# Performance work log

Measured on AMD Instinct MI355X. Metric: run time of the kernel, lower is better.

Reference implementation:

```python
import jax, jax.numpy as jnp
import numpy as np

N_NODES = 50000
N_EDGES = 800000
D_FEAT = 128
HIDDEN = 128
BERT_DIM = 768
BATCH = 4096
MAX_ENT = 20
COMB = BERT_DIM + HIDDEN  # 896


def setup_inputs() -> dict:
    key = jax.random.key(0)
    ks = jax.random.split(key, 12)
    article_bert_embeddings = jax.random.normal(ks[0], (BATCH, BERT_DIM), dtype=jnp.float32)
    x = jax.random.normal(ks[1], (N_NODES, D_FEAT), dtype=jnp.float32)
    edge_index = jax.random.randint(ks[2], (2, N_EDGES), 0, N_NODES, dtype=jnp.int64)
    entity_map = jax.random.randint(ks[3], (BATCH, MAX_ENT), 0, N_NODES, dtype=jnp.int64)
    pad = jax.random.uniform(ks[4], (BATCH, MAX_ENT)) < 0.3
    entity_map = jnp.where(pad, jnp.int64(-1), entity_map)
    s = 1.0 / np.sqrt(D_FEAT)
    W1 = jax.random.normal(ks[5], (D_FEAT, HIDDEN), dtype=jnp.float32) * s
    b1 = jnp.zeros((HIDDEN,), dtype=jnp.float32)
    W2 = jax.random.normal(ks[6], (HIDDEN, HIDDEN), dtype=jnp.float32) * (1.0 / np.sqrt(HIDDEN))
    b2 = jnp.zeros((HIDDEN,), dtype=jnp.float32)
    fc1_w = jax.random.normal(ks[7], (COMB, COMB // 2), dtype=jnp.float32) * (1.0 / np.sqrt(COMB))
    fc1_b = jnp.zeros((COMB // 2,), dtype=jnp.float32)
    fc2_w = jax.random.normal(ks[8], (COMB // 2, 1), dtype=jnp.float32) * (1.0 / np.sqrt(COMB // 2))
    fc2_b = jnp.zeros((1,), dtype=jnp.float32)
    return dict(article_bert_embeddings=article_bert_embeddings, x=x,
                edge_index=edge_index, entity_map=entity_map,
                W1=W1, b1=b1, W2=W2, b2=b2,
                fc1_w=fc1_w, fc1_b=fc1_b, fc2_w=fc2_w, fc2_b=fc2_b)


def _gcn_norm(edge_index, n_nodes):
    # add self loops (PyG GCNConv default) and compute symmetric normalization
    loops = jnp.arange(n_nodes, dtype=edge_index.dtype)
    src = jnp.concatenate([edge_index[0], loops])
    dst = jnp.concatenate([edge_index[1], loops])
    deg = jax.ops.segment_sum(jnp.ones_like(dst, dtype=jnp.float32), dst, num_segments=n_nodes)
    dinv = jnp.where(deg > 0, jax.lax.rsqrt(deg), 0.0)
    norm = dinv[src] * dinv[dst]  # [E+N]
    return src, dst, norm


def _gcn_conv(h, W, b, src, dst, norm, n_nodes):
    h = h @ W                                   # [N, H] transform first (cheaper)
    msg = h[src] * norm[:, None]                # [E+N, H] gather
    out = jax.ops.segment_sum(msg, dst, num_segments=n_nodes)
    return out + b


def reference(article_bert_embeddings, x, edge_index, entity_map,
              W1, b1, W2, b2, fc1_w, fc1_b, fc2_w, fc2_b):
    n = x.shape[0]
    src, dst, norm = _gcn_norm(edge_index, n)
    # GNN (dropout in eval mode = identity)
    h = jax.nn.relu(_gcn_conv(x, W1, b1, src, dst, norm, n))
    h = jax.nn.relu(_gcn_conv(h, W2, b2, src, dst, norm, n))
    # ragged mean over entity lists (-1 = padding), fully vectorized
    mask = entity_map >= 0                           # [B, M]
    safe_ids = jnp.where(mask, entity_map, 0)
    gathered = h[safe_ids] * mask[..., None]         # [B, M, H]
    cnt = jnp.maximum(mask.sum(axis=1, keepdims=True).astype(h.dtype), 1.0)
    batch_gnn = gathered.sum(axis=1) / cnt           # [B, H]; rows w/ no entities stay 0
    combined = jnp.concatenate([article_bert_embeddings, batch_gnn], axis=1)
    z = jax.nn.relu(combined @ fc1_w + fc1_b)
    logits = z @ fc2_w + fc2_b
    return jax.nn.sigmoid(logits)
```

## Files before the change

kernel.cpp:

```cpp
#include <hip/hip_runtime.h>
#include <math.h>

typedef __bf16 bf16_t;
typedef __bf16 bfrag8 __attribute__((ext_vector_type(8)));
typedef float  facc4  __attribute__((ext_vector_type(4)));
typedef float  f32x2  __attribute__((ext_vector_type(2)));

#define NBUCK 512
#define BCAP  4096

__device__ inline unsigned short f2b(float x) {
    unsigned int u = __float_as_uint(x);
    unsigned int r = (u + 0x7fffu + ((u >> 16) & 1u)) >> 16;
    return (unsigned short)r;
}
__device__ inline unsigned int pack2(float lo, float hi) {
    return (unsigned int)f2b(lo) | ((unsigned int)f2b(hi) << 16);
}
__device__ inline float blo(unsigned int q) { return __uint_as_float(q << 16); }
__device__ inline float bhi(unsigned int q) { return __uint_as_float(q & 0xffff0000u); }

#if __has_builtin(__builtin_amdgcn_cvt_pk_f32_fp8) && __has_builtin(__builtin_amdgcn_cvt_pk_fp8_f32)
#define HW_FP8 1
#endif

__device__ inline f32x2 fp8pair_dec(unsigned short v) {
#ifdef HW_FP8
    return __builtin_amdgcn_cvt_pk_f32_fp8((int)(unsigned int)v, false);
#else
    f32x2 r;
    unsigned char b0 = (unsigned char)(v & 0xff), b1 = (unsigned char)(v >> 8);
    {
        int e = (b0 >> 3) & 0xf, m = b0 & 7;
        float mag = e ? ldexpf(8.f + m, e - 10) : ldexpf((float)m, -9);
        r.x = (b0 & 0x80) ? -mag : mag;
    }
    {
        int e = (b1 >> 3) & 0xf, m = b1 & 7;
        float mag = e ? ldexpf(8.f + m, e - 10) : ldexpf((float)m, -9);
        r.y = (b1 & 0x80) ? -mag : mag;
    }
    return r;
#endif
}
__device__ inline unsigned char fp8_enc(float x) {
#ifdef HW_FP8
    return (unsigned char)(__builtin_amdgcn_cvt_pk_fp8_f32(x, x, 0, false) & 0xff);
#else
    unsigned char s = (x < 0.f) ? 0x80 : 0;
    float ax = fabsf(x);
    if (!(ax > 0.f)) return s;
    if (ax >= 448.f) return s | 0x7e;
    if (ax < 0.015625f) {
        int q = (int)rintf(ax * 512.f);
        return s | (unsigned char)q;
    }
    int e; float m = frexpf(ax, &e);
    int q = (int)rintf(m * 16.f);
    int E = e - 1;
    if (q == 16) { q = 8; ++E; }
    if (E > 8) return s | 0x7e;
    return s | (unsigned char)(((E + 7) << 3) | (q - 8));
#endif
}

__device__ inline int bucket_of(int d, int N) {
    return (int)(((long long)d * NBUCK) / N);
}


__device__ inline void bin2_body(char* smem, const int* __restrict__ src,
                                 const int* __restrict__ dst,
                                 int* __restrict__ bcnt,
                                 unsigned int* __restrict__ ebuf,
                                 int E, int N, int bb) {
    unsigned int* sorted = (unsigned int*)smem;
    int* hist   = (int*)(smem + 16384);
    int* lstart = (int*)(smem + 18432);
    int* gbase  = (int*)(smem + 20480);
    int* sm     = (int*)(smem + 22528);
    int tid = threadIdx.x;
    int base = bb * 4096;
    int cnt = min(4096, E - base);
    hist[tid] = 0; hist[tid + 256] = 0;
    __syncthreads();
    unsigned int mye[16]; int myb[16];
#pragma unroll
    for (int i = 0; i < 16; ++i) {
        int idx = i * 256 + tid;
        myb[i] = -1;
        if (idx < cnt) {
            int e = base + idx;
            int s = src[e], d = dst[e];
            mye[i] = ((unsigned int)s << 16) | (unsigned int)d;
            int b = bucket_of(d, N);
            myb[i] = b;
            atomicAdd(&hist[b], 1);
        }
    }
    __syncthreads();
    int p0 = hist[2 * tid], p1 = hist[2 * tid + 1];
    sm[tid] = p0 + p1;
    __syncthreads();
    for (int off = 1; off < 256; off <<= 1) {
        int x = (tid >= off) ? sm[tid - off] : 0;
        __syncthreads();
        sm[tid] += x;
        __syncthreads();
    }
    int excl = sm[tid] - (p0 + p1);
    lstart[2 * tid] = excl;
    lstart[2 * tid + 1] = excl + p0;
    __syncthreads();
    hist[tid] = lstart[tid]; hist[tid + 256] = lstart[tid + 256];
    __syncthreads();
#pragma unroll
    for (int i = 0; i < 16; ++i) {
        if (myb[i] >= 0) {
            int pos = atomicAdd(&hist[myb[i]], 1);
            sorted[pos] = mye[i];
        }
    }
    __syncthreads();
    for (int b = tid; b < NBUCK; b += 256) {
        int c = hist[b] - lstart[b];
        gbase[b] = (c > 0) ? atomicAdd(&bcnt[b], c) : 0;
    }
    __syncthreads();
    for (int idx = tid; idx < cnt; idx += 256) {
        unsigned int v = sorted[idx];
        int b = bucket_of((int)(v & 0xffffu), N);
        ebuf[(size_t)b * BCAP + gbase[b] + (idx - lstart[b])] = v;
    }
}

__device__ inline void build2_body(char* smem, const unsigned int* __restrict__ ebuf,
                                   const int* __restrict__ bcnt,
                                   int* __restrict__ offs,
                                   float* __restrict__ dinv,
                                   unsigned short* __restrict__ csr,
                                   int N, int E, int b) {
    unsigned short* seg = (unsigned short*)smem;
    int* cnt_l  = (int*)(smem + 8192);
    int* scan_l = (int*)(smem + 8704);
    int* curs   = (int*)(smem + 9216);
    int* smr    = (int*)(smem + 9728);
    int tid = threadIdx.x;
    int part = 0;
    for (int j = tid; j < b; j += 256) part += bcnt[j];
    smr[tid] = part;
    __syncthreads();
    for (int off = 128; off > 0; off >>= 1) {
        if (tid < off) smr[tid] += smr[tid + off];
        __syncthreads();
    }
    int base = smr[0];
    int lo = (int)(((long long)b * N + NBUCK - 1) / NBUCK);
    int cnt = bcnt[b];
    int nrange = (int)(((long long)(b + 1) * N + NBUCK - 1) / NBUCK) - lo;
    if (b == 0 && tid == 0) offs[N] = E;
    if (tid < 128) cnt_l[tid] = 0;
    __syncthreads();
    for (int i = tid; i < cnt; i += 256) {
        unsigned int v = ebuf[(size_t)b * BCAP + i];
        atomicAdd(&cnt_l[(int)(v & 0xffffu) - lo], 1);
    }
    __syncthreads();
    if (tid < 128) scan_l[tid] = cnt_l[tid];
    __syncthreads();
    for (int off = 1; off < 128; off <<= 1) {
        int x = 0;
        if (tid < 128 && tid >= off) x = scan_l[tid - off];
        __syncthreads();
        if (tid < 128) scan_l[tid] += x;
        __syncthreads();
    }
    if (tid < 128) {
        int excl = scan_l[tid] - cnt_l[tid];
        curs[tid] = excl;
        if (tid < nrange) {
            offs[lo + tid] = base + excl;
            dinv[lo + tid] = rsqrtf((float)(cnt_l[tid] + 1));
        }
    }
    __syncthreads();
    for (int i = tid; i < cnt; i += 256) {
        unsigned int v = ebuf[(size_t)b * BCAP + i];
        int d = (int)(v & 0xffffu) - lo;
        int p = atomicAdd(&curs[d], 1);
        seg[p] = (unsigned short)(v >> 16);
    }
    __syncthreads();
    for (int i = tid; i < cnt; i += 256) csr[base + i] = seg[i];
}

__device__ inline void gemm1_body(char* smem, const float* __restrict__ A,
                                  const bf16_t* __restrict__ Bt,
                                  unsigned char* __restrict__ out8, int M, int bb) {
    bf16_t* As = (bf16_t*)smem;
    bf16_t* Bs = (bf16_t*)(smem + 17408);
    int t = threadIdx.x;
    int wave = t >> 6, lane = t & 63, quad = lane >> 4, l16 = lane & 15;
    int r0 = bb * 64;
#pragma unroll
    for (int i = 0; i < 4; ++i) {
        int chunk = t + i * 256;
        int row = chunk >> 4, c8 = (chunk & 15) << 3;
        int gr = r0 + row;
        float4 a0 = make_float4(0.f, 0.f, 0.f, 0.f), a1 = a0;
        if (gr < M) {
            a0 = *(const float4*)&A[(size_t)gr * 128 + c8];
            a1 = *(const float4*)&A[(size_t)gr * 128 + c8 + 4];
        }
        *(uint4*)&As[row * 136 + c8] =
            make_uint4(pack2(a0.x, a0.y), pack2(a0.z, a0.w),
                       pack2(a1.x, a1.y), pack2(a1.z, a1.w));
    }
#pragma unroll
    for (int i = 0; i < 8; ++i) {
        int chunk = t + i * 256;
        int row = chunk >> 4, c8 = (chunk & 15) << 3;
        *(uint4*)&Bs[row * 136 + c8] = *(const uint4*)&Bt[row * 128 + c8];
    }
    __syncthreads();

    facc4 acc[8];
#pragma unroll
    for (int nt = 0; nt < 8; ++nt) acc[nt] = (facc4){0.f, 0.f, 0.f, 0.f};
    int arow = (wave << 4) + l16;
#pragma unroll
    for (int ks = 0; ks < 4; ++ks) {
        int kk = ks * 32 + quad * 8;
        bfrag8 af = *(const bfrag8*)&As[arow * 136 + kk];
#pragma unroll
        for (int nt = 0; nt < 8; ++nt) {
            bfrag8 bf = *(const bfrag8*)&Bs[(nt * 16 + l16) * 136 + kk];
            acc[nt] = __builtin_amdgcn_mfma_f32_16x16x32_bf16(af, bf, acc[nt], 0, 0, 0);
        }
    }
    __syncthreads();
    unsigned char* f8t = (unsigned char*)As;
    int wrow0 = (wave << 4) + quad * 4;
#pragma unroll
    for (int r = 0; r < 4; ++r) {
        int row = wrow0 + r;
#pragma unroll
        for (int nt = 0; nt < 8; ++nt)
            f8t[row * 128 + nt * 16 + l16] = fp8_enc(acc[nt][r]);
    }
    __syncthreads();
#pragma unroll
    for (int i = 0; i < 2; ++i) {
        int idx = t + i * 256;
        int row = idx >> 3, cc = (idx & 7) << 4;
        int gr = r0 + row;
        if (gr < M) *(uint4*)&out8[(size_t)gr * 128 + cc] = *(const uint4*)&f8t[row * 128 + cc];
    }
}

__global__ __launch_bounds__(256) void k_bin_gemm(const int* __restrict__ src,
                                                  const int* __restrict__ dst,
                                                  int* __restrict__ bcnt,
                                                  unsigned int* __restrict__ ebuf,
                                                  int E, int N,
                                                  const float* __restrict__ A,
                                                  const bf16_t* __restrict__ Bt,
                                                  unsigned char* __restrict__ out8,
                                                  int nbin) {
    __shared__ __align__(16) char smem[52224];
    if ((int)blockIdx.x < nbin)
        bin2_body(smem, src, dst, bcnt, ebuf, E, N, blockIdx.x);
    else
        gemm1_body(smem, A, Bt, out8, N, blockIdx.x - nbin);
}

__global__ __launch_bounds__(256) void k_build_gemm(const unsigned int* __restrict__ ebuf,
                                                    const int* __restrict__ bcnt,
                                                    int* __restrict__ offs,
                                                    float* __restrict__ dinv,
                                                    unsigned short* __restrict__ csr,
                                                    int N, int E,
                                                    const float* __restrict__ A,
                                                    const bf16_t* __restrict__ Bt,
                                                    unsigned char* __restrict__ out8,
                                                    int tile0) {
    __shared__ __align__(16) char smem[52224];
    if ((int)blockIdx.x < NBUCK)
        build2_body(smem, ebuf, bcnt, offs, dinv, csr, N, E, blockIdx.x);
    else
        gemm1_body(smem, A, Bt, out8, N, blockIdx.x - NBUCK + tile0);
}

__global__ __launch_bounds__(256) void k_prep(const float* __restrict__ bert,
                                              unsigned int* __restrict__ bertb, int n8,
                                              const float* __restrict__ W1,
                                              unsigned short* __restrict__ w1t,
                                              const float* __restrict__ W2,
                                              unsigned short* __restrict__ w2t,
                                              const float* __restrict__ Wf,
                                              unsigned short* __restrict__ fwt,
                                              int* __restrict__ bcnt,
                                              float* __restrict__ logacc) {
    __shared__ float tile[64][65];
    int ncvt = (n8 + 255) / 256;
    int bb = blockIdx.x, tid = threadIdx.x;
    if (bb < ncvt) {
        int i = bb * 256 + tid;
        if (i >= n8) return;
        const float4* p = (const float4*)bert + (size_t)i * 2;
        float4 a = p[0], b = p[1];
        uint4 o;
        o.x = pack2(a.x, a.y);
        o.y = pack2(a.z, a.w);
        o.z = pack2(b.x, b.y);
        o.w = pack2(b.z, b.w);
        ((uint4*)bertb)[i] = o;
        return;
    }
    bb -= ncvt;
    if (bb < 128) {
        int i = bb * 256 + tid;
        const float* W = (i < 16384) ? W1 : W2;
        unsigned short* Wt = (i < 16384) ? w1t : w2t;
        int idx = i & 16383;
        int n = idx >> 7, k = idx & 127;
        Wt[idx] = f2b(W[k * 128 + n]);
        return;
    }
    bb -= 128;
    if (bb < 98) {
        int n0 = (bb % 7) * 64, k0 = (bb / 7) * 64;
#pragma unroll
        for (int i = 0; i < 16; ++i) {
            int idx = i * 256 + tid;
            int r = idx >> 6, c = idx & 63;
            tile[r][c] = Wf[(size_t)(k0 + r) * 448 + n0 + c];
        }
        __syncthreads();
#pragma unroll
        for (int i = 0; i < 16; ++i) {
            int idx = i * 256 + tid;
            int c = idx >> 6, r = idx & 63;
            fwt[(size_t)(n0 + c) * 896 + k0 + r] = f2b(tile[r][c]);
        }
        return;
    }
    if (tid < 256) { bcnt[tid] = 0; bcnt[tid + 256] = 0; }
#pragma unroll
    for (int i = 0; i < 16; ++i) logacc[i * 256 + tid] = 0.f;
}

__global__ __launch_bounds__(256) void k_aggmm(const unsigned short* __restrict__ hx8,
                                               const unsigned short* __restrict__ csr,
                                               const int* __restrict__ offs,
                                               const float* __restrict__ dinv,
                                               const float* __restrict__ bias1,
                                               const bf16_t* __restrict__ W2t,
                                               unsigned char* __restrict__ out8, int N) {
    __shared__ bf16_t As[64 * 136];
    __shared__ bf16_t Bs[128 * 136];
    int t = threadIdx.x;
    int wave = t >> 6, lane = t & 63, quad = lane >> 4, l16 = lane & 15;
    int r0 = blockIdx.x * 64;
#pragma unroll
    for (int i = 0; i < 8; ++i) {
        int chunk = t + i * 256;
        int row = chunk >> 4, c8 = (chunk & 15) << 3;
        *(uint4*)&Bs[row * 136 + c8] = *(const uint4*)&W2t[row * 128 + c8];
    }
    float2 b2v = *(const float2*)&bias1[lane * 2];
    for (int i = 0; i < 16; ++i) {
        int row = (wave << 4) + i;
        int node = r0 + row;
        float v0 = 0.f, v1 = 0.f;
        if (node < N) {
            float di = dinv[node];
            f32x2 sf = fp8pair_dec(hx8[(size_t)node * 64 + lane]);
            float acc0 = sf.x * di, acc1 = sf.y * di;
            int s0 = offs[node], s1 = offs[node + 1];
            for (int eb = s0; eb < s1; eb += 64) {
                int nloc = min(64, s1 - eb);
                int en = 0; float dvl = 0.f;
                if (lane < nloc) { en = (int)csr[eb + lane]; dvl = dinv[en]; }
                int j = 0;
                for (; j + 16 <= nloc; j += 16) {
                    int sid[16]; float dv[16]; unsigned short g[16];
#pragma unroll
                    for (int u = 0; u < 16; ++u) {
                        sid[u] = __shfl(en, j + u, 64);
                        dv[u]  = __shfl(dvl, j + u, 64);
                    }
#pragma unroll
                    for (int u = 0; u < 16; ++u) g[u] = hx8[(size_t)sid[u] * 64 + lane];
#pragma unroll
                    for (int u = 0; u < 16; ++u) {
                        f32x2 d = fp8pair_dec(g[u]);
                        acc0 += d.x * dv[u]; acc1 += d.y * dv[u];
                    }
                }
                for (; j + 4 <= nloc; j += 4) {
                    int sid[4]; float dv[4]; unsigned short g[4];
#pragma unroll
                    for (int u = 0; u < 4; ++u) {
                        sid[u] = __shfl(en, j + u, 64);
                        dv[u]  = __shfl(dvl, j + u, 64);
                    }
#pragma unroll
                    for (int u = 0; u < 4; ++u) g[u] = hx8[(size_t)sid[u] * 64 + lane];
#pragma unroll
                    for (int u = 0; u < 4; ++u) {
                        f32x2 d = fp8pair_dec(g[u]);
                        acc0 += d.x * dv[u]; acc1 += d.y * dv[u];
                    }
                }
                for (; j < nloc; ++j) {
                    int sn = __shfl(en, j, 64);
                    float dv = __shfl(dvl, j, 64);
                    f32x2 d = fp8pair_dec(hx8[(size_t)sn * 64 + lane]);
                    acc0 += d.x * dv; acc1 += d.y * dv;
                }
            }
            v0 = fmaxf(acc0 * di + b2v.x, 0.f);
            v1 = fmaxf(acc1 * di + b2v.y, 0.f);
        }
        *(unsigned int*)&As[row * 136 + lane * 2] = pack2(v0, v1);
    }
    __syncthreads();
    facc4 acc[8];
#pragma unroll
    for (int nt = 0; nt < 8; ++nt) acc[nt] = (facc4){0.f, 0.f, 0.f, 0.f};
    int arow = (wave << 4) + l16;
#pragma unroll
    for (int ks = 0; ks < 4; ++ks) {
        int kk = ks * 32 + quad * 8;
        bfrag8 af = *(const bfrag8*)&As[arow * 136 + kk];
#pragma unroll
        for (int nt = 0; nt < 8; ++nt) {
            bfrag8 bf = *(const bfrag8*)&Bs[(nt * 16 + l16) * 136 + kk];
            acc[nt] = __builtin_amdgcn_mfma_f32_16x16x32_bf16(af, bf, acc[nt], 0, 0, 0);
        }
    }
    __syncthreads();
    unsigned char* f8t = (unsigned char*)As;
    int wrow0 = (wave << 4) + quad * 4;
#pragma unroll
    for (int r = 0; r < 4; ++r) {
        int row = wrow0 + r;
        float sc = dinv[min(r0 + row, N - 1)];
#pragma unroll
        for (int nt = 0; nt < 8; ++nt)
            f8t[row * 128 + nt * 16 + l16] = fp8_enc(acc[nt][r] * sc);
    }
    __syncthreads();
#pragma unroll
    for (int i = 0; i < 2; ++i) {
        int idx = t + i * 256;
        int row = idx >> 3, cc = (idx & 7) << 4;
        int gr = r0 + row;
        if (gr < N) *(uint4*)&out8[(size_t)gr * 128 + cc] = *(const uint4*)&f8t[row * 128 + cc];
    }
}

__global__ __launch_bounds__(256) void k_agg_b(const unsigned short* __restrict__ hx8,
                                               const unsigned short* __restrict__ csr,
                                               const int* __restrict__ offs,
                                               const float* __restrict__ dinv,
                                               const float* __restrict__ bias,
                                               unsigned int* __restrict__ out, int N) {
    int node = blockIdx.x * 4 + (threadIdx.x >> 6);
    int lane = threadIdx.x & 63;
    if (node >= N) return;
    float di = dinv[node];
    f32x2 sf = fp8pair_dec(hx8[(size_t)node * 64 + lane]);
    float acc0 = sf.x, acc1 = sf.y;
    int s0 = offs[node], s1 = offs[node + 1];
    for (int base = s0; base < s1; base += 64) {
        int nloc = min(64, s1 - base);
        int en = 0;
        if (lane < nloc) en = (int)csr[base + lane];
        int j = 0;
        for (; j + 16 <= nloc; j += 16) {
            int sid[16]; unsigned short g[16];
#pragma unroll
            for (int u = 0; u < 16; ++u) sid[u] = __shfl(en, j + u, 64);
#pragma unroll
            for (int u = 0; u < 16; ++u) g[u] = hx8[(size_t)sid[u] * 64 + lane];
#pragma unroll
            for (int u = 0; u < 16; ++u) { f32x2 d = fp8pair_dec(g[u]); acc0 += d.x; acc1 += d.y; }
        }
        for (; j + 4 <= nloc; j += 4) {
            int sid[4]; unsigned short g[4];
#pragma unroll
            for (int u = 0; u < 4; ++u) sid[u] = __shfl(en, j + u, 64);
#pragma unroll
            for (int u = 0; u < 4; ++u) g[u] = hx8[(size_t)sid[u] * 64 + lane];
#pragma unroll
            for (int u = 0; u < 4; ++u) { f32x2 d = fp8pair_dec(g[u]); acc0 += d.x; acc1 += d.y; }
        }
        for (; j < nloc; ++j) {
            int srcn = __shfl(en, j, 64);
            f32x2 d = fp8pair_dec(hx8[(size_t)srcn * 64 + lane]);
            acc0 += d.x; acc1 += d.y;
        }
    }
    float2 bb = *(const float2*)&bias[lane * 2];
    float v0 = fmaxf(acc0 * di + bb.x, 0.f);
    float v1 = fmaxf(acc1 * di + bb.y, 0.f);
    out[(size_t)node * 64 + lane] = pack2(v0, v1);
}

__global__ __launch_bounds__(256) void k_pool_b(const unsigned int* __restrict__ h,
                                                const int* __restrict__ ent,
                                                unsigned int* __restrict__ out) {
    int r = blockIdx.x * 4 + (threadIdx.x >> 6);
    int lane = threadIdx.x & 63;
    float a0 = 0.f, a1 = 0.f;
    int cnt = 0;
#pragma unroll
    for (int m = 0; m < 20; ++m) {
        int id = ent[r * 20 + m];
        if (id >= 0) {
            unsigned int q = h[(size_t)id * 64 + lane];
            a0 += blo(q); a1 += bhi(q); cnt++;
        }
    }
    float inv = 1.f / (float)max(cnt, 1);
    out[(size_t)r * 64 + lane] = pack2(a0 * inv, a1 * inv);
}

__global__ __launch_bounds__(256) void k_mlp1_mfma(const bf16_t* __restrict__ bertb,
                                                   const bf16_t* __restrict__ gnnb,
                                                   const bf16_t* __restrict__ fwt,
                                                   const float* __restrict__ fb,
                                                   const float* __restrict__ w2,
                                                   float* __restrict__ logacc) {
    __shared__ bf16_t As[64 * 136];
    __shared__ bf16_t Bs[64 * 136];
    int t = threadIdx.x;
    int wave = t >> 6, lane = t & 63, quad = lane >> 4, l16 = lane & 15;
    int r0 = blockIdx.x * 64, c0 = blockIdx.y * 64;
    facc4 acc[4];
#pragma unroll
    for (int nt = 0; nt < 4; ++nt) acc[nt] = (facc4){0.f, 0.f, 0.f, 0.f};

    for (int ks = 0; ks < 7; ++ks) {
#pragma unroll
        for (int i = 0; i < 4; ++i) {
            int chunk = t + i * 256;
            int row = chunk >> 4, c8 = (chunk & 15) << 3;
            int gr = r0 + row;
            const bf16_t* srcp = (ks < 6) ? &bertb[(size_t)gr * 768 + ks * 128 + c8]
                                          : &gnnb[(size_t)gr * 128 + c8];
            *(uint4*)&As[row * 136 + c8] = *(const uint4*)srcp;
        }
#pragma unroll
        for (int i = 0; i < 4; ++i) {
            int chunk = t + i * 256;
            int row = chunk >> 4, c8 = (chunk & 15) << 3;
            *(uint4*)&Bs[row * 136 + c8] =
                *(const uint4*)&fwt[(size_t)(c0 + row) * 896 + ks * 128 + c8];
        }
        __syncthreads();
        int arow = (wave << 4) + l16;
#pragma unroll
        for (int sub = 0; sub < 4; ++sub) {
            int kk = sub * 32 + quad * 8;
            bfrag8 af = *(const bfrag8*)&As[arow * 136 + kk];
#pragma unroll
            for (int nt = 0; nt < 4; ++nt) {
                bfrag8 bf = *(const bfrag8*)&Bs[(nt * 16 + l16) * 136 + kk];
                acc[nt] = __builtin_amdgcn_mfma_f32_16x16x32_bf16(af, bf, acc[nt], 0, 0, 0);
            }
        }
        __syncthreads();
    }
    int rbase = r0 + (wave << 4) + quad * 4;
    float part[4] = {0.f, 0.f, 0.f, 0.f};
#pragma unroll
    for (int nt = 0; nt < 4; ++nt) {
        int col = c0 + nt * 16 + l16;
        float bb = fb[col];
        float ww = w2[col];
#pragma unroll
        for (int r = 0; r < 4; ++r)
            part[r] += fmaxf(acc[nt][r] + bb, 0.f) * ww;
    }
#pragma unroll
    for (int m = 8; m >= 1; m >>= 1) {
#pragma unroll
        for (int r = 0; r < 4; ++r) part[r] += __shfl_xor(part[r], m, 64);
    }
    if (l16 == 0) {
#pragma unroll
        for (int r = 0; r < 4; ++r) atomicAdd(&logacc[rbase + r], part[r]);
    }
}

__global__ void k_sig(const float* __restrict__ logacc, const float* __restrict__ b,
                      float* __restrict__ out, int B) {
    int i = blockIdx.x * 256 + threadIdx.x;
    if (i < B) out[i] = 1.f / (1.f + expf(-(logacc[i] + b[0])));
}

extern "C" void kernel_launch(void* const* d_in, const int* in_sizes, int n_in,
                              void* d_out, int out_size, void* d_ws, size_t ws_size,
                              hipStream_t stream) {
    const float* bert = (const float*)d_in[0];
    const float* x    = (const float*)d_in[1];
    const int*   ei   = (const int*)d_in[2];
    const int*   ent  = (const int*)d_in[3];
    const float* W1   = (const float*)d_in[4];
    const float* b1   = (const float*)d_in[5];
    const float* W2   = (const float*)d_in[6];
    const float* b2   = (const float*)d_in[7];
    const float* fc1w = (const float*)d_in[8];
    const float* fc1b = (const float*)d_in[9];
    const float* fc2w = (const float*)d_in[10];
    const float* fc2b = (const float*)d_in[11];
    float* out = (float*)d_out;

    const int N = in_sizes[1] / 128;
    const int E = in_sizes[2] / 2;
    const int B = in_sizes[0] / 768;

    const int* srcv = ei;
    const int* dstv = ei + E;

    char* wsp = (char*)d_ws;
    size_t off = 0;
    auto alloc = [&](size_t bytes) -> void* {
        void* p = wsp + off;
        off += (bytes + 255) & ~(size_t)255;
        return p;
    };
    float* dinv   = (float*)alloc((size_t)N * 4);
    int*   offs   = (int*)alloc((size_t)(N + 1) * 4);
    int*   bcnt   = (int*)alloc(NBUCK * 4);
    float* logacc = (float*)alloc((size_t)B * 4);
    unsigned int*   ebuf  = (unsigned int*)alloc((size_t)NBUCK * BCAP * 4);
    unsigned short* csr16 = (unsigned short*)alloc((size_t)E * 2);
    bf16_t* bertb = (bf16_t*)alloc((size_t)B * 768 * 2);
    bf16_t* w1t   = (bf16_t*)alloc(128 * 128 * 2);
    bf16_t* w2t   = (bf16_t*)alloc(128 * 128 * 2);
    bf16_t* fwt   = (bf16_t*)alloc((size_t)896 * 448 * 2);
    unsigned char* g8a = (unsigned char*)alloc((size_t)N * 128);
    unsigned char* g8b = (unsigned char*)alloc((size_t)N * 128);
    bf16_t* hbuf  = (bf16_t*)alloc((size_t)N * 128 * 2);
    bf16_t* gnnb  = (bf16_t*)alloc((size_t)B * 128 * 2);
    (void)ws_size; (void)n_in; (void)out_size;

    int nb8 = B * 768 / 8;
    int ncvt = (nb8 + 255) / 256;
    int nprep = ncvt + 128 + 98 + 1;
    int nbin = (E + 4095) / 4096;
    int gb = (N + 63) / 64;
    int g1a = gb / 2, g1b = gb - g1a;

    k_prep<<<nprep, 256, 0, stream>>>(bert, (unsigned int*)bertb, nb8,
                                      W1, (unsigned short*)w1t, W2, (unsigned short*)w2t,
                                      fc1w, (unsigned short*)fwt, bcnt, logacc);
    k_bin_gemm<<<nbin + g1a, 256, 0, stream>>>(srcv, dstv, bcnt, ebuf, E, N,
                                               x, w1t, g8a, nbin);
    k_build_gemm<<<NBUCK + g1b, 256, 0, stream>>>(ebuf, bcnt, offs, dinv, csr16, N, E,
                                                  x, w1t, g8a, g1a);
    k_aggmm<<<gb, 256, 0, stream>>>((const unsigned short*)g8a, csr16, offs, dinv, b1,
                                    w2t, g8b, N);
    k_agg_b<<<(N + 3) / 4, 256, 0, stream>>>((const unsigned short*)g8b, csr16, offs, dinv, b2,
                                             (unsigned int*)hbuf, N);
    k_pool_b<<<B / 4, 256, 0, stream>>>((const unsigned int*)hbuf, ent, (unsigned int*)gnnb);
    k_mlp1_mfma<<<dim3(B / 64, 7), 256, 0, stream>>>(bertb, gnnb, fwt, fc1b, fc2w, logacc);
    k_sig<<<(B + 255) / 256, 256, 0, stream>>>(logacc, fc2b, out, B);
}
```

Before: 242.4 us.

## Split fused layer-1 aggregation+GEMM into separate aggregation and GEMM kernels

Replaces the fused kernel that aggregated 64 nodes per block and then ran a 128x128 MFMA GEMM with two kernels. The first is a one-wave-per-node aggregation kernel that writes bf16 rows to a buffer; the second is a standalone GEMM that reads those rows and writes fp8 output. The aim is better load balance and more parallelism for the irregular gather, since each block no longer serializes 16 nodes per wave before the GEMM. In exchange it adds an extra kernel launch and a round trip of the bf16 intermediate through global memory.

```diff
diff --git a/kernel.cpp b/kernel.cpp
--- a/kernel.cpp
+++ b/kernel.cpp
@@ -350,82 +350,32 @@
     for (int i = 0; i < 16; ++i) logacc[i * 256 + tid] = 0.f;
 }
 
-__global__ __launch_bounds__(256) void k_aggmm(const unsigned short* __restrict__ hx8,
-                                               const unsigned short* __restrict__ csr,
-                                               const int* __restrict__ offs,
-                                               const float* __restrict__ dinv,
-                                               const float* __restrict__ bias1,
-                                               const bf16_t* __restrict__ W2t,
-                                               unsigned char* __restrict__ out8, int N) {
+__global__ __launch_bounds__(256) void k_gemm_nn128(const bf16_t* __restrict__ A,
+                                                    const bf16_t* __restrict__ Bt,
+                                                    const float* __restrict__ rs,
+                                                    unsigned char* __restrict__ out8, int M) {
     __shared__ bf16_t As[64 * 136];
     __shared__ bf16_t Bs[128 * 136];
     int t = threadIdx.x;
     int wave = t >> 6, lane = t & 63, quad = lane >> 4, l16 = lane & 15;
     int r0 = blockIdx.x * 64;
 #pragma unroll
+    for (int i = 0; i < 4; ++i) {
+        int chunk = t + i * 256;
+        int row = chunk >> 4, c8 = (chunk & 15) << 3;
+        int gr = r0 + row;
+        uint4 v = make_uint4(0u, 0u, 0u, 0u);
+        if (gr < M) v = *(const uint4*)&A[(size_t)gr * 128 + c8];
+        *(uint4*)&As[row * 136 + c8] = v;
+    }
+#pragma unroll
     for (int i = 0; i < 8; ++i) {
         int chunk = t + i * 256;
         int row = chunk >> 4, c8 = (chunk & 15) << 3;
-        *(uint4*)&Bs[row * 136 + c8] = *(const uint4*)&W2t[row * 128 + c8];
-    }
-    float2 b2v = *(const float2*)&bias1[lane * 2];
-    for (int i = 0; i < 16; ++i) {
-        int row = (wave << 4) + i;
-        int node = r0 + row;
-        float v0 = 0.f, v1 = 0.f;
-        if (node < N) {
-            float di = dinv[node];
-            f32x2 sf = fp8pair_dec(hx8[(size_t)node * 64 + lane]);
-            float acc0 = sf.x * di, acc1 = sf.y * di;
-            int s0 = offs[node], s1 = offs[node + 1];
-            for (int eb = s0; eb < s1; eb += 64) {
-                int nloc = min(64, s1 - eb);
-                int en = 0; float dvl = 0.f;
-                if (lane < nloc) { en = (int)csr[eb + lane]; dvl = dinv[en]; }
-                int j = 0;
-                for (; j + 16 <= nloc; j += 16) {
-                    int sid[16]; float dv[16]; unsigned short g[16];
-#pragma unroll
-                    for (int u = 0; u < 16; ++u) {
-                        sid[u] = __shfl(en, j + u, 64);
-                        dv[u]  = __shfl(dvl, j + u, 64);
-                    }
-#pragma unroll
-                    for (int u = 0; u < 16; ++u) g[u] = hx8[(size_t)sid[u] * 64 + lane];
-#pragma unroll
-                    for (int u = 0; u < 16; ++u) {
-                        f32x2 d = fp8pair_dec(g[u]);
-                        acc0 += d.x * dv[u]; acc1 += d.y * dv[u];
-                    }
-                }
-                for (; j + 4 <= nloc; j += 4) {
-                    int sid[4]; float dv[4]; unsigned short g[4];
-#pragma unroll
-                    for (int u = 0; u < 4; ++u) {
-                        sid[u] = __shfl(en, j + u, 64);
-                        dv[u]  = __shfl(dvl, j + u, 64);
-                    }
-#pragma unroll
-                    for (int u = 0; u < 4; ++u) g[u] = hx8[(size_t)sid[u] * 64 + lane];
-#pragma unroll
-                    for (int u = 0; u < 4; ++u) {
-                        f32x2 d = fp8pair_dec(g[u]);
-                        acc0 += d.x * dv[u]; acc1 += d.y * dv[u];
-                    }
-                }
-                for (; j < nloc; ++j) {
-                    int sn = __shfl(en, j, 64);
-                    float dv = __shfl(dvl, j, 64);
-                    f32x2 d = fp8pair_dec(hx8[(size_t)sn * 64 + lane]);
-                    acc0 += d.x * dv; acc1 += d.y * dv;
-                }
-            }
-            v0 = fmaxf(acc0 * di + b2v.x, 0.f);
-            v1 = fmaxf(acc1 * di + b2v.y, 0.f);
-        }
-        *(unsigned int*)&As[row * 136 + lane * 2] = pack2(v0, v1);
-    }
-    __syncthreads();
+        *(uint4*)&Bs[row * 136 + c8] = *(const uint4*)&Bt[row * 128 + c8];
+    }
+    __syncthreads();
+
     facc4 acc[8];
 #pragma unroll
     for (int nt = 0; nt < 8; ++nt) acc[nt] = (facc4){0.f, 0.f, 0.f, 0.f};
@@ -446,7 +396,7 @@
 #pragma unroll
     for (int r = 0; r < 4; ++r) {
         int row = wrow0 + r;
-        float sc = dinv[min(r0 + row, N - 1)];
+        float sc = rs[min(r0 + row, M - 1)];
 #pragma unroll
         for (int nt = 0; nt < 8; ++nt)
             f8t[row * 128 + nt * 16 + l16] = fp8_enc(acc[nt][r] * sc);
@@ -457,8 +407,69 @@
         int idx = t + i * 256;
         int row = idx >> 3, cc = (idx & 7) << 4;
         int gr = r0 + row;
-        if (gr < N) *(uint4*)&out8[(size_t)gr * 128 + cc] = *(const uint4*)&f8t[row * 128 + cc];
-    }
+        if (gr < M) *(uint4*)&out8[(size_t)gr * 128 + cc] = *(const uint4*)&f8t[row * 128 + cc];
+    }
+}
+
+__global__ __launch_bounds__(256) void k_agg_w(const unsigned short* __restrict__ hx8,
+                                               const unsigned short* __restrict__ csr,
+                                               const int* __restrict__ offs,
+                                               const float* __restrict__ dinv,
+                                               const float* __restrict__ bias,
+                                               unsigned int* __restrict__ out, int N) {
+    int node = blockIdx.x * 4 + (threadIdx.x >> 6);
+    int lane = threadIdx.x & 63;
+    if (node >= N) return;
+    float di = dinv[node];
+    f32x2 sf = fp8pair_dec(hx8[(size_t)node * 64 + lane]);
+    float acc0 = sf.x * di, acc1 = sf.y * di;
+    int s0 = offs[node], s1 = offs[node + 1];
+    for (int base = s0; base < s1; base += 64) {
+        int nloc = min(64, s1 - base);
+        int en = 0; float dvl = 0.f;
+        if (lane < nloc) { en = (int)csr[base + lane]; dvl = dinv[en]; }
+        int j = 0;
+        for (; j + 16 <= nloc; j += 16) {
+            int sid[16]; float dv[16]; unsigned short g[16];
+#pragma unroll
+            for (int u = 0; u < 16; ++u) {
+                sid[u] = __shfl(en, j + u, 64);
+                dv[u]  = __shfl(dvl, j + u, 64);
+            }
+#pragma unroll
+            for (int u = 0; u < 16; ++u) g[u] = hx8[(size_t)sid[u] * 64 + lane];
+#pragma unroll
+            for (int u = 0; u < 16; ++u) {
+                f32x2 d = fp8pair_dec(g[u]);
+                acc0 += d.x * dv[u]; acc1 += d.y * dv[u];
+            }
+        }
+        for (; j + 4 <= nloc; j += 4) {
+            int sid[4]; float dv[4]; unsigned short g[4];
+#pragma unroll
+            for (int u = 0; u < 4; ++u) {
+                sid[u] = __shfl(en, j + u, 64);
+                dv[u]  = __shfl(dvl, j + u, 64);
+            }
+#pragma unroll
+            for (int u = 0; u < 4; ++u) g[u] = hx8[(size_t)sid[u] * 64 + lane];
+#pragma unroll
+            for (int u = 0; u < 4; ++u) {
+                f32x2 d = fp8pair_dec(g[u]);
+                acc0 += d.x * dv[u]; acc1 += d.y * dv[u];
+            }
+        }
+        for (; j < nloc; ++j) {
+            int srcn = __shfl(en, j, 64);
+            float dv = __shfl(dvl, j, 64);
+            f32x2 d = fp8pair_dec(hx8[(size_t)srcn * 64 + lane]);
+            acc0 += d.x * dv; acc1 += d.y * dv;
+        }
+    }
+    float2 bb = *(const float2*)&bias[lane * 2];
+    float v0 = fmaxf(acc0 * di + bb.x, 0.f);
+    float v1 = fmaxf(acc1 * di + bb.y, 0.f);
+    out[(size_t)node * 64 + lane] = pack2(v0, v1);
 }
 
 __global__ __launch_bounds__(256) void k_agg_b(const unsigned short* __restrict__ hx8,
@@ -663,8 +674,9 @@
                                                x, w1t, g8a, nbin);
     k_build_gemm<<<NBUCK + g1b, 256, 0, stream>>>(ebuf, bcnt, offs, dinv, csr16, N, E,
                                                   x, w1t, g8a, g1a);
-    k_aggmm<<<gb, 256, 0, stream>>>((const unsigned short*)g8a, csr16, offs, dinv, b1,
-                                    w2t, g8b, N);
+    k_agg_w<<<(N + 3) / 4, 256, 0, stream>>>((const unsigned short*)g8a, csr16, offs, dinv, b1,
+                                             (unsigned int*)hbuf, N);
+    k_gemm_nn128<<<gb, 256, 0, stream>>>(hbuf, w2t, dinv, g8b, N);
     k_agg_b<<<(N + 3) / 4, 256, 0, stream>>>((const unsigned short*)g8b, csr16, offs, dinv, b2,
                                              (unsigned int*)hbuf, N);
     k_pool_b<<<B / 4, 256, 0, stream>>>((const unsigned int*)hbuf, ent, (unsigned int*)gnnb);
```

New measurement: 212.6 us, median of 2. -12.3%, faster.
